# Performance work log

Measured on AMD Instinct MI355X. Metric: run time of the kernel, lower is better.

The kernel has to match this reference:

```python
import jax, jax.numpy as jnp
import numpy as np

K = 5  # Chebyshev order (K+1 = 6 terms)


def cheb_graph_conv(x, gso, W, b):
    # x: [B, N, F_in], gso: [B, N, N], W: [K+1, F_in, F_out], b: [F_out]
    # Fused recurrence + weighted accumulate (same math as stack+einsum).
    t_prev2 = x
    t_prev = jnp.einsum('bij,bjf->bif', gso, x)
    out = jnp.einsum('bif,fo->bio', t_prev2, W[0]) + jnp.einsum('bif,fo->bio', t_prev, W[1])
    for k in range(2, K + 1):
        t = 2.0 * jnp.einsum('bij,bjf->bif', gso, t_prev) - t_prev2
        out = out + jnp.einsum('bif,fo->bio', t, W[k])
        t_prev2, t_prev = t_prev, t
    return out + b


def layernorm2d(x, gamma, beta, eps=1e-5):
    # LayerNorm over the last TWO dims (normalized_shape=[N, D])
    mu = jnp.mean(x, axis=(-2, -1), keepdims=True)
    var = jnp.var(x, axis=(-2, -1), keepdims=True)
    return (x - mu) / jnp.sqrt(var + eps) * gamma + beta


def lrelu(x):
    return jnp.where(x >= 0, x, 0.2 * x)


def setup_inputs() -> dict:
    key = jax.random.key(0)
    ks = jax.random.split(key, 24)
    B, N, D = 64, 512, 64
    f32 = jnp.float32
    A = jax.random.normal(ks[0], (B, N, N), f32) / jnp.sqrt(jnp.asarray(N, f32))
    X = jax.random.normal(ks[1], (B, N, N), f32)
    s_in = 1.0 / np.sqrt(N)
    s_d = 1.0 / np.sqrt(D)
    W1 = jax.random.normal(ks[2], (K + 1, N, D), f32) * s_in
    b1 = jax.random.normal(ks[3], (D,), f32) * s_in
    W2 = jax.random.normal(ks[4], (K + 1, D, D), f32) * s_d
    b2 = jax.random.normal(ks[5], (D,), f32) * s_d
    W3 = jax.random.normal(ks[6], (K + 1, D, D), f32) * s_d
    b3 = jax.random.normal(ks[7], (D,), f32) * s_d
    g1 = jnp.ones((N, D), f32); bt1 = jnp.zeros((N, D), f32)
    g2 = jnp.ones((N, D), f32); bt2 = jnp.zeros((N, D), f32)
    dZ = (D + D) * 2  # 256
    s_z = 1.0 / np.sqrt(dZ)
    p1w = jax.random.normal(ks[8], (dZ, D), f32) * s_z
    p1b = jax.random.normal(ks[9], (D,), f32) * s_z
    p2w = jax.random.normal(ks[10], (D, D), f32) * s_d
    p2b = jax.random.normal(ks[11], (D,), f32) * s_d
    p3w = jax.random.normal(ks[12], (D, 4), f32) * s_d
    p3b = jax.random.normal(ks[13], (4,), f32) * s_d
    s1w = jax.random.normal(ks[14], (dZ, D), f32) * s_z
    s1b = jax.random.normal(ks[15], (D,), f32) * s_z
    s2w = jax.random.normal(ks[16], (D, D), f32) * s_d
    s2b = jax.random.normal(ks[17], (D,), f32) * s_d
    p4w = jax.random.normal(ks[18], (D, 2), f32) * s_d
    p4b = jax.random.normal(ks[19], (2,), f32) * s_d
    return dict(A=A, X=X, W1=W1, b1=b1, W2=W2, b2=b2, W3=W3, b3=b3,
                g1=g1, bt1=bt1, g2=g2, bt2=bt2,
                p1w=p1w, p1b=p1b, p2w=p2w, p2b=p2b, p3w=p3w, p3b=p3b,
                s1w=s1w, s1b=s1b, s2w=s2w, s2b=s2b, p4w=p4w, p4b=p4b)


def reference(A, X, W1, b1, W2, b2, W3, b3, g1, bt1, g2, bt2,
              p1w, p1b, p2w, p2b, p3w, p3b, s1w, s1b, s2w, s2b, p4w, p4b):
    B, N, _ = X.shape
    # start_gcn -> norm1 -> relu
    h = jax.nn.relu(layernorm2d(cheb_graph_conv(X, A, W1, b1), g1, bt1))  # [B,N,64]
    z1 = jnp.mean(h, axis=1, keepdims=True)       # [B,1,64]
    z2 = jnp.max(h, axis=1, keepdims=True)        # [B,1,64]
    Z = jnp.concatenate([z1, z2], axis=2)         # [B,1,128]
    # bottom_gcn -> norm2 -> relu
    h = jax.nn.relu(layernorm2d(cheb_graph_conv(h, A, W2, b2), g2, bt2))  # [B,N,64]
    z1 = jnp.mean(h, axis=1, keepdims=True)
    z2 = jnp.max(h, axis=1, keepdims=True)
    Z = jnp.concatenate([Z, z1, z2], axis=2)      # [B,1,256]
    # end_gcn, outer product, relu, normalize (zero diag then symmetrize)
    X0 = cheb_graph_conv(h, A, W3, b3)            # [B,N,64]
    AE = jax.nn.relu(jnp.einsum('bif,bjf->bij', X0, X0))  # [B,N,N]
    eye = jnp.eye(N, dtype=AE.dtype)
    AE = AE * (1.0 - eye)                          # fill_diagonal_(0)
    AE = 0.5 * (AE + jnp.swapaxes(AE, 1, 2))       # symmetrize (diag stays 0)
    # heads
    Zf = Z.reshape(B, -1)                          # [B,256]
    q = lrelu(Zf @ p1w + p1b)
    q = lrelu(q @ p2w + p2b)
    out_class = jax.nn.sigmoid(q @ p3w + p3b)      # [B,4]
    s = lrelu(Zf @ s1w + s1b)
    s = lrelu(s @ s2w + s2b)
    scanner_class = jax.nn.log_softmax(s @ p4w + p4b, axis=1)  # [B,2]
    return AE, out_class, scanner_class
```

## Files before the change

kernel.cpp:

```cpp
#include <hip/hip_runtime.h>

#define NN 512
#define DD 64
#define BB 64
#define ND (NN * DD)

static const long BND = (long)BB * ND;

typedef __bf16 bf16x8 __attribute__((ext_vector_type(8)));
typedef float  f32x4  __attribute__((ext_vector_type(4)));

__device__ __forceinline__ float bf2f(unsigned short u) {
    return __uint_as_float(((unsigned int)u) << 16);
}
__device__ __forceinline__ void cvt4(const float4& x, ushort4& h, ushort4& l) {
    __bf16 h0 = (__bf16)x.x, h1 = (__bf16)x.y, h2 = (__bf16)x.z, h3 = (__bf16)x.w;
    __bf16 l0 = (__bf16)(x.x - (float)h0);
    __bf16 l1 = (__bf16)(x.y - (float)h1);
    __bf16 l2 = (__bf16)(x.z - (float)h2);
    __bf16 l3 = (__bf16)(x.w - (float)h3);
    h = make_ushort4(__builtin_bit_cast(unsigned short, h0),
                     __builtin_bit_cast(unsigned short, h1),
                     __builtin_bit_cast(unsigned short, h2),
                     __builtin_bit_cast(unsigned short, h3));
    l = make_ushort4(__builtin_bit_cast(unsigned short, l0),
                     __builtin_bit_cast(unsigned short, l1),
                     __builtin_bit_cast(unsigned short, l2),
                     __builtin_bit_cast(unsigned short, l3));
}
__device__ __forceinline__ bf16x8 ld_bf8(const unsigned short* p) {
    int4 v = *reinterpret_cast<const int4*>(p);
    return __builtin_bit_cast(bf16x8, v);
}
__device__ __forceinline__ f32x4 mfma16(bf16x8 a, bf16x8 b, f32x4 c) {
    return __builtin_amdgcn_mfma_f32_16x16x32_bf16(a, b, c, 0, 0, 0);
}
__device__ __forceinline__ int swzW4(int r, int c) {
    return r * 64 + (((c >> 1) ^ (r & 7)) << 3) + ((c & 1) << 2);
}
__device__ __forceinline__ int swzR(int r, int oct) {
    return r * 64 + ((oct ^ (r & 7)) << 3);
}

template <bool HAS_VM, bool HAS_Z, bool HAS_BIAS, bool OUT_ROW>
__global__ __launch_bounds__(512) void gemm_mfma(
    const float* __restrict__ A, int lda, long aBatch,
    const float* __restrict__ U, long uBatch, long uZ,
    const float* __restrict__ Vm, const float* __restrict__ Zt,
    const float* __restrict__ bias, float alpha, float beta, int kdim,
    float* __restrict__ out, long outZ, int nz)
{
    const int nwg = gridDim.x;
    const int lid = (blockIdx.x & 7) * (nwg >> 3) + (blockIdx.x >> 3);
    const int z   = lid % nz;
    const int t2  = lid / nz;
    const int i0  = (t2 & 7) << 6;
    const int b   = t2 >> 3;

    const float* __restrict__ Ab = A + (long)b * aBatch;
    const float* __restrict__ Ub = U + (long)b * uBatch + (long)z * uZ;

    __shared__ __align__(16) unsigned short sAh[4096];
    __shared__ __align__(16) unsigned short sAl[4096];
    __shared__ __align__(16) unsigned short sBh[4096];
    __shared__ __align__(16) unsigned short sBl[4096];

    const int t = threadIdx.x;
    const int w = t >> 6, lane = t & 63;
    const int wr = w >> 1, wc = w & 1;
    const int lr = lane & 15, lg = lane >> 4;

    f32x4 acc[2];
    acc[0] = f32x4{0.f, 0.f, 0.f, 0.f};
    acc[1] = f32x4{0.f, 0.f, 0.f, 0.f};

    const int steps = kdim >> 6;
    float4 ra[2], rb[2];

#pragma unroll
    for (int l = 0; l < 2; ++l) {
        int q = t + l * 512, r = q >> 4, c = q & 15;
        ra[l] = *reinterpret_cast<const float4*>(Ab + (long)(i0 + r) * lda + c * 4);
        rb[l] = *reinterpret_cast<const float4*>(Ub + (long)r * kdim + c * 4);
    }

    for (int s = 0; s < steps; ++s) {
        if (s) __syncthreads();
#pragma unroll
        for (int l = 0; l < 2; ++l) {
            int q = t + l * 512, r = q >> 4, c = q & 15;
            int idx = swzW4(r, c);
            ushort4 h4, l4;
            cvt4(ra[l], h4, l4);
            *reinterpret_cast<ushort4*>(&sAh[idx]) = h4;
            *reinterpret_cast<ushort4*>(&sAl[idx]) = l4;
            cvt4(rb[l], h4, l4);
            *reinterpret_cast<ushort4*>(&sBh[idx]) = h4;
            *reinterpret_cast<ushort4*>(&sBl[idx]) = l4;
        }
        __syncthreads();
        if (s + 1 < steps) {
            const int k0n = (s + 1) << 6;
#pragma unroll
            for (int l = 0; l < 2; ++l) {
                int q = t + l * 512, r = q >> 4, c = q & 15;
                ra[l] = *reinterpret_cast<const float4*>(Ab + (long)(i0 + r) * lda + k0n + c * 4);
                rb[l] = *reinterpret_cast<const float4*>(Ub + (long)r * kdim + k0n + c * 4);
            }
        }
#pragma unroll
        for (int c2 = 0; c2 < 2; ++c2) {
            const int oct = c2 * 4 + lg;
            const int arow = wr * 16 + lr;
            bf16x8 a_h = ld_bf8(&sAh[swzR(arow, oct)]);
            bf16x8 a_l = ld_bf8(&sAl[swzR(arow, oct)]);
            bf16x8 b_h[2], b_l[2];
#pragma unroll
            for (int n = 0; n < 2; ++n) {
                int col = wc * 32 + n * 16 + lr;
                b_h[n] = ld_bf8(&sBh[swzR(col, oct)]);
                b_l[n] = ld_bf8(&sBl[swzR(col, oct)]);
            }
#pragma unroll
            for (int n = 0; n < 2; ++n) {
                acc[n] = mfma16(a_h, b_h[n], acc[n]);
                acc[n] = mfma16(a_h, b_l[n], acc[n]);
                acc[n] = mfma16(a_l, b_h[n], acc[n]);
            }
        }
    }

    const long cOff = (long)b * ND;
    const long oOff = (long)z * outZ + cOff;
    const int nb = i0 + wr * 16 + lg * 4;
#pragma unroll
    for (int n = 0; n < 2; ++n) {
        const int f = wc * 32 + n * 16 + lr;
        float4 v;
        v.x = alpha * acc[n][0]; v.y = alpha * acc[n][1];
        v.z = alpha * acc[n][2]; v.w = alpha * acc[n][3];
        if (HAS_VM) {
            float4 mv = *reinterpret_cast<const float4*>(Vm + cOff + (long)f * NN + nb);
            v.x += beta * mv.x; v.y += beta * mv.y; v.z += beta * mv.z; v.w += beta * mv.w;
        }
        if (HAS_Z) {
            float4 zz = *reinterpret_cast<const float4*>(Zt + cOff + (long)f * NN + nb);
            v.x += zz.x; v.y += zz.y; v.z += zz.z; v.w += zz.w;
        }
        if (HAS_BIAS) {
            float bf = bias[f];
            v.x += bf; v.y += bf; v.z += bf; v.w += bf;
        }
        if (OUT_ROW) {
            float* __restrict__ outb = out + cOff;
            outb[(long)(nb + 0) * DD + f] = v.x;
            outb[(long)(nb + 1) * DD + f] = v.y;
            outb[(long)(nb + 2) * DD + f] = v.z;
            outb[(long)(nb + 3) * DD + f] = v.w;
        } else {
            *reinterpret_cast<float4*>(out + oOff + (long)f * NN + nb) = v;
        }
    }
}

__global__ __launch_bounds__(256) void outer_v14(
    const float* __restrict__ X0, float* __restrict__ AE)
{
    const int b = blockIdx.z;
    const int j0 = blockIdx.x * 64, i0 = blockIdx.y * 64;
    const float* __restrict__ Xb = X0 + (long)b * ND;

    __shared__ __align__(16) unsigned short sIh[4096];
    __shared__ __align__(16) unsigned short sIl[4096];
    __shared__ __align__(16) unsigned short sJh[4096];
    __shared__ __align__(16) unsigned short sJl[4096];

    const int t = threadIdx.x;
    const int w = t >> 6, lane = t & 63;
    const int wr = w >> 1, wc = w & 1;
    const int lr = lane & 15, lg = lane >> 4;

#pragma unroll
    for (int l = 0; l < 4; ++l) {
        int q = t + l * 256;
        int r = q >> 4, c = q & 15;
        int idx = swzW4(r, c);
        ushort4 h4, l4;
        float4 vi = *reinterpret_cast<const float4*>(Xb + (long)(i0 + r) * DD + c * 4);
        cvt4(vi, h4, l4);
        *reinterpret_cast<ushort4*>(&sIh[idx]) = h4;
        *reinterpret_cast<ushort4*>(&sIl[idx]) = l4;
        float4 vj = *reinterpret_cast<const float4*>(Xb + (long)(j0 + r) * DD + c * 4);
        cvt4(vj, h4, l4);
        *reinterpret_cast<ushort4*>(&sJh[idx]) = h4;
        *reinterpret_cast<ushort4*>(&sJl[idx]) = l4;
    }
    __syncthreads();

    f32x4 acc[2][2];
#pragma unroll
    for (int m = 0; m < 2; ++m)
#pragma unroll
        for (int n = 0; n < 2; ++n) acc[m][n] = f32x4{0.f, 0.f, 0.f, 0.f};

#pragma unroll
    for (int c2 = 0; c2 < 2; ++c2) {
        const int oct = c2 * 4 + lg;
        bf16x8 a_h[2], a_l[2], b_h[2], b_l[2];
#pragma unroll
        for (int m = 0; m < 2; ++m) {
            int row = wr * 32 + m * 16 + lr;
            a_h[m] = ld_bf8(&sIh[swzR(row, oct)]);
            a_l[m] = ld_bf8(&sIl[swzR(row, oct)]);
            int col = wc * 32 + m * 16 + lr;
            b_h[m] = ld_bf8(&sJh[swzR(col, oct)]);
            b_l[m] = ld_bf8(&sJl[swzR(col, oct)]);
        }
#pragma unroll
        for (int m = 0; m < 2; ++m)
#pragma unroll
            for (int n = 0; n < 2; ++n) {
                acc[m][n] = mfma16(a_h[m], b_h[n], acc[m][n]);
                acc[m][n] = mfma16(a_h[m], b_l[n], acc[m][n]);
                acc[m][n] = mfma16(a_l[m], b_h[n], acc[m][n]);
            }
    }

    float* __restrict__ AEb = AE + (long)b * NN * NN;
#pragma unroll
    for (int m = 0; m < 2; ++m) {
        const int ib = i0 + wr * 32 + m * 16 + lg * 4;
#pragma unroll
        for (int n = 0; n < 2; ++n) {
            const int jc = j0 + wc * 32 + n * 16 + lr;
#pragma unroll
            for (int jj = 0; jj < 4; ++jj) {
                float v = fmaxf(acc[m][n][jj], 0.f);
                if (ib + jj == jc) v = 0.f;
                AEb[(long)(ib + jj) * NN + jc] = v;
            }
        }
    }
}

__global__ __launch_bounds__(256) void ln_pool(
    const float* __restrict__ pre, const float* __restrict__ gamma,
    const float* __restrict__ beta, float* __restrict__ h,
    float* __restrict__ zfeat, int zoff)
{
    const int b = blockIdx.x;
    const float* __restrict__ p = pre + (long)b * ND;
    const int t = threadIdx.x;

    float s = 0.f, s2 = 0.f;
    for (int i = t * 4; i < ND; i += 1024) {
        float4 v = *reinterpret_cast<const float4*>(p + i);
        s  += v.x + v.y + v.z + v.w;
        s2 += v.x * v.x + v.y * v.y + v.z * v.z + v.w * v.w;
    }
#pragma unroll
    for (int off = 32; off > 0; off >>= 1) {
        s  += __shfl_down(s, off, 64);
        s2 += __shfl_down(s2, off, 64);
    }
    __shared__ float red[8];
    if ((t & 63) == 0) { red[(t >> 6) * 2] = s; red[(t >> 6) * 2 + 1] = s2; }
    __syncthreads();
    __shared__ float mu_s, rstd_s;
    if (t == 0) {
        float ts  = red[0] + red[2] + red[4] + red[6];
        float ts2 = red[1] + red[3] + red[5] + red[7];
        float mu  = ts * (1.f / ND);
        float var = ts2 * (1.f / ND) - mu * mu;
        mu_s = mu; rstd_s = rsqrtf(var + 1e-5f);
    }
    __syncthreads();
    const float mu = mu_s, rstd = rstd_s;

    const int f4 = (t & 15) * 4, nt = t >> 4;
    float sum4[4] = {0.f, 0.f, 0.f, 0.f};
    float max4[4] = {0.f, 0.f, 0.f, 0.f};
    for (int n = nt; n < NN; n += 16) {
        float4 g4 = *reinterpret_cast<const float4*>(gamma + (long)n * DD + f4);
        float4 be = *reinterpret_cast<const float4*>(beta  + (long)n * DD + f4);
        float4 v;
        v.x = fmaxf((p[(long)(f4 + 0) * NN + n] - mu) * rstd * g4.x + be.x, 0.f);
        v.y = fmaxf((p[(long)(f4 + 1) * NN + n] - mu) * rstd * g4.y + be.y, 0.f);
        v.z = fmaxf((p[(long)(f4 + 2) * NN + n] - mu) * rstd * g4.z + be.z, 0.f);
        v.w = fmaxf((p[(long)(f4 + 3) * NN + n] - mu) * rstd * g4.w + be.w, 0.f);
        *reinterpret_cast<float4*>(h + (long)b * ND + (long)n * DD + f4) = v;
        sum4[0] += v.x; sum4[1] += v.y; sum4[2] += v.z; sum4[3] += v.w;
        max4[0] = fmaxf(max4[0], v.x); max4[1] = fmaxf(max4[1], v.y);
        max4[2] = fmaxf(max4[2], v.z); max4[3] = fmaxf(max4[3], v.w);
    }
    __shared__ float rs[16][64], rm[16][64];
#pragma unroll
    for (int j = 0; j < 4; ++j) { rs[nt][f4 + j] = sum4[j]; rm[nt][f4 + j] = max4[j]; }
    __syncthreads();
    if (t < 64) {
        float ss = 0.f, mm = 0.f;
#pragma unroll
        for (int k = 0; k < 16; ++k) { ss += rs[k][t]; mm = fmaxf(mm, rm[k][t]); }
        zfeat[b * 256 + zoff + t]      = ss * (1.f / NN);
        zfeat[b * 256 + zoff + 64 + t] = mm;
    }
}

__global__ void transW(const float* __restrict__ W, float* __restrict__ Wt,
                       int kdim, int total)
{
    int o = blockIdx.x * 256 + threadIdx.x;
    if (o >= total) return;
    int per = 64 * kdim;
    int zz = o / per, r = o % per;
    int f = r / kdim, k = r % kdim;
    Wt[o] = W[((long)zz * kdim + k) * 64 + f];
}

__global__ __launch_bounds__(64) void heads(
    const float* __restrict__ zfeat,
    const float* __restrict__ p1w, const float* __restrict__ p1b,
    const float* __restrict__ p2w, const float* __restrict__ p2b,
    const float* __restrict__ p3w, const float* __restrict__ p3b,
    const float* __restrict__ s1w, const float* __restrict__ s1b,
    const float* __restrict__ s2w, const float* __restrict__ s2b,
    const float* __restrict__ p4w, const float* __restrict__ p4b,
    float* __restrict__ outc, float* __restrict__ outs)
{
    const int b = blockIdx.x, t = threadIdx.x;
    __shared__ float zf[256], v1[64], v2[64], lg[2];
    for (int i = t; i < 256; i += 64) zf[i] = zfeat[b * 256 + i];
    __syncthreads();

    float a = p1b[t];
    for (int z = 0; z < 256; ++z) a = fmaf(zf[z], p1w[z * 64 + t], a);
    v1[t] = a >= 0.f ? a : 0.2f * a;
    __syncthreads();
    float a2 = p2b[t];
    for (int z = 0; z < 64; ++z) a2 = fmaf(v1[z], p2w[z * 64 + t], a2);
    v2[t] = a2 >= 0.f ? a2 : 0.2f * a2;
    __syncthreads();
    if (t < 4) {
        float a3 = p3b[t];
        for (int z = 0; z < 64; ++z) a3 = fmaf(v2[z], p3w[z * 4 + t], a3);
        outc[b * 4 + t] = 1.f / (1.f + expf(-a3));
    }
    __syncthreads();

    float c = s1b[t];
    for (int z = 0; z < 256; ++z) c = fmaf(zf[z], s1w[z * 64 + t], c);
    v1[t] = c >= 0.f ? c : 0.2f * c;
    __syncthreads();
    float c2 = s2b[t];
    for (int z = 0; z < 64; ++z) c2 = fmaf(v1[z], s2w[z * 64 + t], c2);
    v2[t] = c2 >= 0.f ? c2 : 0.2f * c2;
    __syncthreads();
    if (t < 2) {
        float d = p4b[t];
        for (int z = 0; z < 64; ++z) d = fmaf(v2[z], p4w[z * 2 + t], d);
        lg[t] = d;
    }
    __syncthreads();
    if (t < 2) {
        float m = fmaxf(lg[0], lg[1]);
        float lse = m + logf(expf(lg[0] - m) + expf(lg[1] - m));
        outs[b * 2 + t] = lg[t] - lse;
    }
}

extern "C" void kernel_launch(void* const* d_in, const int* in_sizes, int n_in,
                              void* d_out, int out_size, void* d_ws, size_t ws_size,
                              hipStream_t stream)
{
    const float* A   = (const float*)d_in[0];
    const float* X   = (const float*)d_in[1];
    const float* W1  = (const float*)d_in[2];
    const float* b1v = (const float*)d_in[3];
    const float* W2  = (const float*)d_in[4];
    const float* b2v = (const float*)d_in[5];
    const float* W3  = (const float*)d_in[6];
    const float* b3v = (const float*)d_in[7];
    const float* g1  = (const float*)d_in[8];
    const float* bt1 = (const float*)d_in[9];
    const float* g2  = (const float*)d_in[10];
    const float* bt2 = (const float*)d_in[11];
    const float* p1w = (const float*)d_in[12];
    const float* p1b = (const float*)d_in[13];
    const float* p2w = (const float*)d_in[14];
    const float* p2b = (const float*)d_in[15];
    const float* p3w = (const float*)d_in[16];
    const float* p3b = (const float*)d_in[17];
    const float* s1w = (const float*)d_in[18];
    const float* s1b = (const float*)d_in[19];
    const float* s2w = (const float*)d_in[20];
    const float* s2b = (const float*)d_in[21];
    const float* p4w = (const float*)d_in[22];
    const float* p4b = (const float*)d_in[23];

    float* out   = (float*)d_out;
    float* Zs    = out;
    float* bufA  = out + 6 * BND;
    float* bufB  = out + 7 * BND;
    float* ws    = (float*)d_ws;
    float* bufC  = ws;
    float* W1t   = ws;
    float* hbuf  = ws + BND;
    float* zfeat = ws + 2 * BND;
    float* W2t   = ws + 2 * BND + 16384;
    float* W3t   = W2t + 24576;
    float* outc  = out + (long)BB * NN * NN;
    float* outsc = outc + BB * 4;

    const dim3 blk(256), gblk(512);
    const long ABATCH = (long)NN * NN;

    transW<<<dim3((6 * NN * DD + 255) / 256), blk, 0, stream>>>(W1, W1t, NN, 6 * NN * DD);
    transW<<<dim3((6 * DD * DD + 255) / 256), blk, 0, stream>>>(W2, W2t, DD, 6 * DD * DD);
    transW<<<dim3((6 * DD * DD + 255) / 256), blk, 0, stream>>>(W3, W3t, DD, 6 * DD * DD);

    const dim3 gridZ(8 * 64 * 6);
    const dim3 gridC(8 * 64);

    auto cheb = [&](const float* bias, float* xout, bool rowOut) {
        gemm_mfma<false, true, false, false><<<gridC, gblk, 0, stream>>>(
            A, NN, ABATCH, Zs + 5 * BND, (long)ND, 0L, nullptr, Zs + 4 * BND, nullptr,
            2.f, 0.f, NN, bufA, 0L, 1);
        gemm_mfma<true, true, false, false><<<gridC, gblk, 0, stream>>>(
            A, NN, ABATCH, bufA, (long)ND, 0L, Zs + 5 * BND, Zs + 3 * BND, nullptr,
            2.f, -1.f, NN, bufB, 0L, 1);
        gemm_mfma<true, true, false, false><<<gridC, gblk, 0, stream>>>(
            A, NN, ABATCH, bufB, (long)ND, 0L, bufA, Zs + 2 * BND, nullptr,
            2.f, -1.f, NN, bufC, 0L, 1);
        gemm_mfma<true, true, false, false><<<gridC, gblk, 0, stream>>>(
            A, NN, ABATCH, bufC, (long)ND, 0L, bufB, Zs + 1 * BND, nullptr,
            2.f, -1.f, NN, bufA, 0L, 1);
        if (rowOut)
            gemm_mfma<true, true, true, true><<<gridC, gblk, 0, stream>>>(
                A, NN, ABATCH, bufA, (long)ND, 0L, bufC, Zs + 0 * BND, bias,
                1.f, -1.f, NN, xout, 0L, 1);
        else
            gemm_mfma<true, true, true, false><<<gridC, gblk, 0, stream>>>(
                A, NN, ABATCH, bufA, (long)ND, 0L, bufC, Zs + 0 * BND, bias,
                1.f, -1.f, NN, xout, 0L, 1);
    };

    gemm_mfma<false, false, false, false><<<gridZ, gblk, 0, stream>>>(
        X, NN, ABATCH, W1t, 0L, (long)DD * NN, nullptr, nullptr, nullptr,
        1.f, 0.f, NN, Zs, BND, 6);
    cheb(b1v, bufB, false);
    ln_pool<<<dim3(64), blk, 0, stream>>>(bufB, g1, bt1, hbuf, zfeat, 0);

    gemm_mfma<false, false, false, false><<<gridZ, gblk, 0, stream>>>(
        hbuf, DD, (long)ND, W2t, 0L, (long)DD * DD, nullptr, nullptr, nullptr,
        1.f, 0.f, DD, Zs, BND, 6);
    cheb(b2v, bufB, false);
    ln_pool<<<dim3(64), blk, 0, stream>>>(bufB, g2, bt2, hbuf, zfeat, 128);

    gemm_mfma<false, false, false, false><<<gridZ, gblk, 0, stream>>>(
        hbuf, DD, (long)ND, W3t, 0L, (long)DD * DD, nullptr, nullptr, nullptr,
        1.f, 0.f, DD, Zs, BND, 6);
    cheb(b3v, hbuf, true);

    outer_v14<<<dim3(8, 8, 64), blk, 0, stream>>>(hbuf, out);

    heads<<<dim3(64), dim3(64), 0, stream>>>(
        zfeat, p1w, p1b, p2w, p2b, p3w, p3b, s1w, s1b, s2w, s2b, p4w, p4b, outc, outsc);
}
```

Measured before the change: 462.0 us.

## Add two-weight projection GEMM with pre-split bf16 weights to share activation tiles

Adds a new projection kernel that computes two Chebyshev weight outputs per block, so each activation tile is loaded from global memory and split into bf16 hi/lo once per pair of weights instead of once per weight. The weight transpose kernel now also pre-splits weights into bf16 hi/lo halves, which removes the per-tile conversion of weights inside the GEMM. The projection grid shrinks from six z-slices to three, which lowers activation traffic and conversion work but uses more LDS per block and fewer blocks.

```diff
diff --git a/kernel.cpp b/kernel.cpp
--- a/kernel.cpp
+++ b/kernel.cpp
@@ -42,6 +42,128 @@
     return r * 64 + ((oct ^ (r & 7)) << 3);
 }
 
+__global__ __launch_bounds__(512) void gemm_z2(
+    const float* __restrict__ Afp, int lda, long aBatch,
+    const unsigned short* __restrict__ Wh, const unsigned short* __restrict__ Wl,
+    int kdim, float* __restrict__ out, long outZ, int nzp)
+{
+    const int nwg = gridDim.x;
+    const int lid = (blockIdx.x & 7) * (nwg >> 3) + (blockIdx.x >> 3);
+    const int zp  = lid % nzp;
+    const int t2  = lid / nzp;
+    const int i0  = (t2 & 7) << 6;
+    const int b   = t2 >> 3;
+
+    const float* __restrict__ Ab = Afp + (long)b * aBatch;
+    const unsigned short* __restrict__ W0h = Wh + (long)(zp * 2 + 0) * 64 * kdim;
+    const unsigned short* __restrict__ W0l = Wl + (long)(zp * 2 + 0) * 64 * kdim;
+    const unsigned short* __restrict__ W1h = Wh + (long)(zp * 2 + 1) * 64 * kdim;
+    const unsigned short* __restrict__ W1l = Wl + (long)(zp * 2 + 1) * 64 * kdim;
+
+    __shared__ __align__(16) unsigned short sXh[4096];
+    __shared__ __align__(16) unsigned short sXl[4096];
+    __shared__ __align__(16) unsigned short sW0h[4096];
+    __shared__ __align__(16) unsigned short sW0l[4096];
+    __shared__ __align__(16) unsigned short sW1h[4096];
+    __shared__ __align__(16) unsigned short sW1l[4096];
+
+    const int t = threadIdx.x;
+    const int w = t >> 6, lane = t & 63;
+    const int wr = w >> 1, wc = w & 1;
+    const int lr = lane & 15, lg = lane >> 4;
+
+    f32x4 acc[2][2];
+#pragma unroll
+    for (int zz = 0; zz < 2; ++zz)
+#pragma unroll
+        for (int n = 0; n < 2; ++n) acc[zz][n] = f32x4{0.f, 0.f, 0.f, 0.f};
+
+    const int steps = kdim >> 6;
+    const int rW = t >> 3, jW = t & 7;
+    const int widx = rW * 64 + ((jW ^ (rW & 7)) << 3);
+    const long wsrc0 = (long)rW * kdim + jW * 8;
+
+    float4 ra[2];
+    int4 w0h, w0l, w1h, w1l;
+
+#pragma unroll
+    for (int l = 0; l < 2; ++l) {
+        int q = t + l * 512, r = q >> 4, c = q & 15;
+        ra[l] = *reinterpret_cast<const float4*>(Ab + (long)(i0 + r) * lda + c * 4);
+    }
+    w0h = *reinterpret_cast<const int4*>(W0h + wsrc0);
+    w0l = *reinterpret_cast<const int4*>(W0l + wsrc0);
+    w1h = *reinterpret_cast<const int4*>(W1h + wsrc0);
+    w1l = *reinterpret_cast<const int4*>(W1l + wsrc0);
+
+    for (int s = 0; s < steps; ++s) {
+        if (s) __syncthreads();
+#pragma unroll
+        for (int l = 0; l < 2; ++l) {
+            int q = t + l * 512, r = q >> 4, c = q & 15;
+            int idx = swzW4(r, c);
+            ushort4 h4, l4;
+            cvt4(ra[l], h4, l4);
+            *reinterpret_cast<ushort4*>(&sXh[idx]) = h4;
+            *reinterpret_cast<ushort4*>(&sXl[idx]) = l4;
+        }
+        *reinterpret_cast<int4*>(&sW0h[widx]) = w0h;
+        *reinterpret_cast<int4*>(&sW0l[widx]) = w0l;
+        *reinterpret_cast<int4*>(&sW1h[widx]) = w1h;
+        *reinterpret_cast<int4*>(&sW1l[widx]) = w1l;
+        __syncthreads();
+        if (s + 1 < steps) {
+            const int k0n = (s + 1) << 6;
+#pragma unroll
+            for (int l = 0; l < 2; ++l) {
+                int q = t + l * 512, r = q >> 4, c = q & 15;
+                ra[l] = *reinterpret_cast<const float4*>(Ab + (long)(i0 + r) * lda + k0n + c * 4);
+            }
+            w0h = *reinterpret_cast<const int4*>(W0h + wsrc0 + k0n);
+            w0l = *reinterpret_cast<const int4*>(W0l + wsrc0 + k0n);
+            w1h = *reinterpret_cast<const int4*>(W1h + wsrc0 + k0n);
+            w1l = *reinterpret_cast<const int4*>(W1l + wsrc0 + k0n);
+        }
+#pragma unroll
+        for (int c2 = 0; c2 < 2; ++c2) {
+            const int oct = c2 * 4 + lg;
+            const int arow = wr * 16 + lr;
+            bf16x8 a_h = ld_bf8(&sXh[swzR(arow, oct)]);
+            bf16x8 a_l = ld_bf8(&sXl[swzR(arow, oct)]);
+#pragma unroll
+            for (int n = 0; n < 2; ++n) {
+                const int col = wc * 32 + n * 16 + lr;
+                const int ci = swzR(col, oct);
+                bf16x8 b0h = ld_bf8(&sW0h[ci]);
+                bf16x8 b0l = ld_bf8(&sW0l[ci]);
+                acc[0][n] = mfma16(a_h, b0h, acc[0][n]);
+                acc[0][n] = mfma16(a_h, b0l, acc[0][n]);
+                acc[0][n] = mfma16(a_l, b0h, acc[0][n]);
+                bf16x8 b1h = ld_bf8(&sW1h[ci]);
+                bf16x8 b1l = ld_bf8(&sW1l[ci]);
+                acc[1][n] = mfma16(a_h, b1h, acc[1][n]);
+                acc[1][n] = mfma16(a_h, b1l, acc[1][n]);
+                acc[1][n] = mfma16(a_l, b1h, acc[1][n]);
+            }
+        }
+    }
+
+    const long cOff = (long)b * ND;
+    const int nb = i0 + wr * 16 + lg * 4;
+#pragma unroll
+    for (int zz = 0; zz < 2; ++zz) {
+        const long oOff = (long)(zp * 2 + zz) * outZ + cOff;
+#pragma unroll
+        for (int n = 0; n < 2; ++n) {
+            const int f = wc * 32 + n * 16 + lr;
+            float4 v;
+            v.x = acc[zz][n][0]; v.y = acc[zz][n][1];
+            v.z = acc[zz][n][2]; v.w = acc[zz][n][3];
+            *reinterpret_cast<float4*>(out + oOff + (long)f * NN + nb) = v;
+        }
+    }
+}
+
 template <bool HAS_VM, bool HAS_Z, bool HAS_BIAS, bool OUT_ROW>
 __global__ __launch_bounds__(512) void gemm_mfma(
     const float* __restrict__ A, int lda, long aBatch,
@@ -163,7 +285,7 @@
     }
 }
 
-__global__ __launch_bounds__(256) void outer_v14(
+__global__ __launch_bounds__(256) void outer_v15(
     const float* __restrict__ X0, float* __restrict__ AE)
 {
     const int b = blockIdx.z;
@@ -306,15 +428,21 @@
     }
 }
 
-__global__ void transW(const float* __restrict__ W, float* __restrict__ Wt,
-                       int kdim, int total)
+__global__ void transW_split(const float* __restrict__ W,
+                             unsigned short* __restrict__ Wh,
+                             unsigned short* __restrict__ Wl,
+                             int kdim, int total)
 {
     int o = blockIdx.x * 256 + threadIdx.x;
     if (o >= total) return;
     int per = 64 * kdim;
     int zz = o / per, r = o % per;
     int f = r / kdim, k = r % kdim;
-    Wt[o] = W[((long)zz * kdim + k) * 64 + f];
+    float x = W[((long)zz * kdim + k) * 64 + f];
+    __bf16 hb = (__bf16)x;
+    __bf16 lb = (__bf16)(x - (float)hb);
+    Wh[o] = __builtin_bit_cast(unsigned short, hb);
+    Wl[o] = __builtin_bit_cast(unsigned short, lb);
 }
 
 __global__ __launch_bounds__(64) void heads(
@@ -403,22 +531,25 @@
     float* bufB  = out + 7 * BND;
     float* ws    = (float*)d_ws;
     float* bufC  = ws;
-    float* W1t   = ws;
     float* hbuf  = ws + BND;
     float* zfeat = ws + 2 * BND;
-    float* W2t   = ws + 2 * BND + 16384;
-    float* W3t   = W2t + 24576;
+    unsigned short* w1h = (unsigned short*)(zfeat + 16384);
+    unsigned short* w1l = w1h + 6 * NN * DD;
+    unsigned short* w2h = w1l + 6 * NN * DD;
+    unsigned short* w2l = w2h + 6 * DD * DD;
+    unsigned short* w3h = w2l + 6 * DD * DD;
+    unsigned short* w3l = w3h + 6 * DD * DD;
     float* outc  = out + (long)BB * NN * NN;
     float* outsc = outc + BB * 4;
 
     const dim3 blk(256), gblk(512);
     const long ABATCH = (long)NN * NN;
 
-    transW<<<dim3((6 * NN * DD + 255) / 256), blk, 0, stream>>>(W1, W1t, NN, 6 * NN * DD);
-    transW<<<dim3((6 * DD * DD + 255) / 256), blk, 0, stream>>>(W2, W2t, DD, 6 * DD * DD);
-    transW<<<dim3((6 * DD * DD + 255) / 256), blk, 0, stream>>>(W3, W3t, DD, 6 * DD * DD);
-
-    const dim3 gridZ(8 * 64 * 6);
+    transW_split<<<dim3((6 * NN * DD + 255) / 256), blk, 0, stream>>>(W1, w1h, w1l, NN, 6 * NN * DD);
+    transW_split<<<dim3((6 * DD * DD + 255) / 256), blk, 0, stream>>>(W2, w2h, w2l, DD, 6 * DD * DD);
+    transW_split<<<dim3((6 * DD * DD + 255) / 256), blk, 0, stream>>>(W3, w3h, w3l, DD, 6 * DD * DD);
+
+    const dim3 gridZ(8 * 64 * 3);
     const dim3 gridC(8 * 64);
 
     auto cheb = [&](const float* bias, float* xout, bool rowOut) {
@@ -444,24 +575,18 @@
                 1.f, -1.f, NN, xout, 0L, 1);
     };
 
-    gemm_mfma<false, false, false, false><<<gridZ, gblk, 0, stream>>>(
-        X, NN, ABATCH, W1t, 0L, (long)DD * NN, nullptr, nullptr, nullptr,
-        1.f, 0.f, NN, Zs, BND, 6);
+    gemm_z2<<<gridZ, gblk, 0, stream>>>(X, NN, ABATCH, w1h, w1l, NN, Zs, BND, 3);
     cheb(b1v, bufB, false);
     ln_pool<<<dim3(64), blk, 0, stream>>>(bufB, g1, bt1, hbuf, zfeat, 0);
 
-    gemm_mfma<false, false, false, false><<<gridZ, gblk, 0, stream>>>(
-        hbuf, DD, (long)ND, W2t, 0L, (long)DD * DD, nullptr, nullptr, nullptr,
-        1.f, 0.f, DD, Zs, BND, 6);
+    gemm_z2<<<gridZ, gblk, 0, stream>>>(hbuf, DD, (long)ND, w2h, w2l, DD, Zs, BND, 3);
     cheb(b2v, bufB, false);
     ln_pool<<<dim3(64), blk, 0, stream>>>(bufB, g2, bt2, hbuf, zfeat, 128);
 
-    gemm_mfma<false, false, false, false><<<gridZ, gblk, 0, stream>>>(
-        hbuf, DD, (long)ND, W3t, 0L, (long)DD * DD, nullptr, nullptr, nullptr,
-        1.f, 0.f, DD, Zs, BND, 6);
+    gemm_z2<<<gridZ, gblk, 0, stream>>>(hbuf, DD, (long)ND, w3h, w3l, DD, Zs, BND, 3);
     cheb(b3v, hbuf, true);
 
-    outer_v14<<<dim3(8, 8, 64), blk, 0, stream>>>(hbuf, out);
+    outer_v15<<<dim3(8, 8, 64), blk, 0, stream>>>(hbuf, out);
 
     heads<<<dim3(64), dim3(64), 0, stream>>>(
         zfeat, p1w, p1b, p2w, p2b, p3w, p3b, s1w, s1b, s2w, s2b, p4w, p4b, outc, outsc);
```

Result: faster. 445.9 us (-3.5%).
